# Performance work log

Measured on AMD Instinct MI355X. Metric: run time of the kernel, lower is better.

The kernel has to match this reference:

```python
import jax, jax.numpy as jnp
import numpy as np

N = 100000   # nodes
E = 800000   # edges
FEAT = 384   # raw feature dim (match layer input)
IN = 64      # in_dim
H = 64       # hidden_dim


def setup_inputs() -> dict:
    key = jax.random.key(0)
    ks = jax.random.split(key, 9)
    x = jax.random.normal(ks[0], (N, FEAT), dtype=jnp.float32)
    edge_index = jax.random.randint(ks[1], (2, E), 0, N)
    edge_weight = jax.random.uniform(ks[2], (E,), dtype=jnp.float32)
    Wm = jax.random.normal(ks[3], (FEAT, IN), dtype=jnp.float32) * (FEAT ** -0.5)
    bm = jnp.zeros((IN,), dtype=jnp.float32)
    W1 = jax.random.normal(ks[4], (IN, H), dtype=jnp.float32) * (IN ** -0.5)
    b1 = jnp.zeros((H,), dtype=jnp.float32)
    W2 = jax.random.normal(ks[5], (H, H), dtype=jnp.float32) * (H ** -0.5)
    b2 = jnp.zeros((H,), dtype=jnp.float32)
    return {"x": x, "edge_index": edge_index, "edge_weight": edge_weight,
            "Wm": Wm, "bm": bm, "W1": W1, "b1": b1, "W2": W2, "b2": b2}


def _gcn_conv(x, W, b, src, dst, ew, num_nodes):
    """PyG GCNConv: out = D^{-1/2} (A+I) D^{-1/2} (x W) + b."""
    # add self loops with weight 1
    loop = jnp.arange(num_nodes, dtype=src.dtype)
    row = jnp.concatenate([src, loop])          # source (message sender)
    col = jnp.concatenate([dst, loop])          # destination (aggregation target)
    w = jnp.concatenate([ew, jnp.ones((num_nodes,), dtype=x.dtype)])
    # symmetric normalization: deg computed over destination
    deg = jax.ops.segment_sum(w, col, num_segments=num_nodes)
    dinv = jnp.where(deg > 0, jax.lax.rsqrt(deg), 0.0)
    norm = dinv[row] * w * dinv[col]            # [E+N]
    h = x @ W                                   # [N, out]
    msg = h[row] * norm[:, None]                # gather + scale
    out = jax.ops.segment_sum(msg, col, num_segments=num_nodes)  # scatter-add
    return out + b


def reference(x, edge_index, edge_weight, Wm, bm, W1, b1, W2, b2):
    src, dst = edge_index[0], edge_index[1]
    if x.shape[-1] != IN:
        x = x @ Wm + bm                         # match: Linear(384, in_dim)
    h = _gcn_conv(x, W1, b1, src, dst, edge_weight, N)
    h = jax.nn.relu(h)                          # relu between layers only
    out = _gcn_conv(h, W2, b2, src, dst, edge_weight, N)
    return out
```

## Files before the change

kernel.cpp:

```cpp
#include <hip/hip_runtime.h>


#define NN 100000
#define NE 800000
#define BC 32

typedef unsigned short u16;
typedef __attribute__((ext_vector_type(8))) short short8;
typedef __attribute__((ext_vector_type(4))) float f4;
typedef __attribute__((ext_vector_type(8))) unsigned short u16x8;

__device__ __forceinline__ u16 f2b(float f) {
    unsigned int x = __float_as_uint(f);
    x += 0x7fffu + ((x >> 16) & 1u);
    return (u16)(x >> 16);
}
__device__ __forceinline__ float b2f(u16 u) {
    return __uint_as_float(((unsigned int)u) << 16);
}

__global__ __launch_bounds__(256) void mega_k(const int* __restrict__ ei,
                                              const float* __restrict__ ew,
                                              float* __restrict__ deg,
                                              int* __restrict__ count,
                                              int2* __restrict__ e2,
                                              const float* __restrict__ x,
                                              const float* __restrict__ Wm,
                                              const float* __restrict__ bm,
                                              float* __restrict__ t32) {
    __shared__ u16 Blds[4 * 256 * 8];
    int tid = threadIdx.x, bid = blockIdx.x;
    if (bid < 3125) {
        int e = bid * 256 + tid;
        int src = ei[e];
        int dst = ei[NE + e];
        float wv = ew[e];
        atomicAdd(&deg[dst], wv);
        int pos = atomicAdd(&count[dst], 1);
        if (pos < BC)
            e2[(size_t)dst * BC + pos] = make_int2(src, __float_as_int(wv));
        return;
    }
    int wave = tid >> 6, lane = tid & 63;
    int rowtile = (bid - 3125) * 4 + wave;
    bool act = rowtile < 6250;
    int rowbase = (act ? rowtile : 6249) * 16;
    int m = lane & 15, quad = lane >> 4;

    f4 acc[4];
#pragma unroll
    for (int ct = 0; ct < 4; ct++) acc[ct] = 0.0f;
    const short8* Bfrag = (const short8*)Blds;

#pragma unroll
    for (int chunk = 0; chunk < 3; chunk++) {
        for (int idx = tid; idx < 4 * 256; idx += 256) {
            int ktl = idx >> 8, rem = idx & 255;
            int ct = rem >> 6, ln = rem & 63;
            int kb = (chunk * 4 + ktl) * 32 + (ln >> 4) * 8;
            int col = ct * 16 + (ln & 15);
#pragma unroll
            for (int j = 0; j < 8; j++)
                Blds[idx * 8 + j] = f2b(Wm[(size_t)(kb + j) * 64 + col]);
        }
        __syncthreads();
#pragma unroll
        for (int ktl = 0; ktl < 4; ktl++) {
            const f4* p = (const f4*)&x[(size_t)(rowbase + m) * 384 + (chunk * 4 + ktl) * 32 + quad * 8];
            f4 v0 = p[0], v1 = p[1];
            short8 af;
#pragma unroll
            for (int j = 0; j < 4; j++) {
                af[j]     = (short)f2b(v0[j]);
                af[4 + j] = (short)f2b(v1[j]);
            }
#pragma unroll
            for (int ct = 0; ct < 4; ct++)
                acc[ct] = __builtin_amdgcn_mfma_f32_16x16x32_bf16(af, Bfrag[(ktl * 4 + ct) * 64 + lane], acc[ct], 0, 0, 0);
        }
        __syncthreads();
    }

    if (act) {
#pragma unroll
        for (int ct = 0; ct < 4; ct++) {
            int col = ct * 16 + m;
            float bmv = bm[col];
#pragma unroll
            for (int r = 0; r < 4; r++)
                t32[(size_t)(rowbase + quad * 4 + r) * 64 + col] = acc[ct][r] + bmv;
        }
    }
}

__global__ __launch_bounds__(256) void scale_k(const float* __restrict__ deg,
                                               const float* __restrict__ t32,
                                               u16* __restrict__ ts) {
    int tid = threadIdx.x;
    int rt = tid >> 3, ch = tid & 7;
    int row = blockIdx.x * 32 + rt;
    float rsd = rsqrtf(deg[row] + 1.0f);
    const f4* p = (const f4*)&t32[(size_t)row * 64 + ch * 8];
    f4 v0 = p[0], v1 = p[1];
    u16x8 o;
#pragma unroll
    for (int j = 0; j < 4; j++) {
        o[j]     = f2b(rsd * v0[j]);
        o[4 + j] = f2b(rsd * v1[j]);
    }
    ((u16x8*)ts)[(size_t)row * 8 + ch] = o;
}

__device__ __forceinline__ void gatherR(const int2* __restrict__ eb, int cntv, int dst,
                                        const u16* __restrict__ hb, int ch,
                                        float* __restrict__ acc) {
    const int4* eb4 = (const int4*)eb;
    for (int i = 0; i < cntv; i += 8) {
        int4 q[4];
#pragma unroll
        for (int p = 0; p < 4; p++) q[p] = eb4[(i >> 1) + p];
        int s[8];
        float c[8];
#pragma unroll
        for (int p = 0; p < 4; p++) {
            int t0 = i + 2 * p;
            bool v0 = t0 < cntv, v1 = (t0 + 1) < cntv;
            s[2 * p]     = v0 ? q[p].x : dst;
            c[2 * p]     = v0 ? __int_as_float(q[p].y) : 0.0f;
            s[2 * p + 1] = v1 ? q[p].z : dst;
            c[2 * p + 1] = v1 ? __int_as_float(q[p].w) : 0.0f;
        }
        u16x8 hv[8];
#pragma unroll
        for (int t = 0; t < 8; t++)
            hv[t] = *(const u16x8*)&hb[(size_t)s[t] * 64 + ch * 8];
#pragma unroll
        for (int t = 0; t < 8; t++) {
#pragma unroll
            for (int j = 0; j < 8; j++)
                acc[j] = fmaf(c[t], b2f(hv[t][j]), acc[j]);
        }
    }
}

__device__ __forceinline__ void fillW(u16* Wlds, const float* __restrict__ W, int tid) {
    for (int idx = tid; idx < 2 * 256; idx += 256) {
        int kt = idx >> 8, rem = idx & 255;
        int ct = rem >> 6, ln = rem & 63;
        int kb = kt * 32 + (ln >> 4) * 8;
        int col = ct * 16 + (ln & 15);
#pragma unroll
        for (int j = 0; j < 8; j++)
            Wlds[idx * 8 + j] = f2b(W[(size_t)(kb + j) * 64 + col]);
    }
}

__global__ __launch_bounds__(256) void g1gemm_k(const int2* __restrict__ e2,
                                                const int* __restrict__ count,
                                                const float* __restrict__ deg,
                                                const u16* __restrict__ ts,
                                                const float* __restrict__ W1,
                                                const float* __restrict__ b1,
                                                u16* __restrict__ aggb) {
    __shared__ u16 Wlds[4096];
    __shared__ u16 Atile[32][72];
    __shared__ float rsds[32];
    int tid = threadIdx.x;
    fillW(Wlds, W1, tid);

    int rt = tid >> 3, ch = tid & 7;
    int dst = blockIdx.x * 32 + rt;
    int cntv = min(count[dst], BC);
    float rsdd = rsqrtf(deg[dst] + 1.0f);
    u16x8 hs = *(const u16x8*)&ts[(size_t)dst * 64 + ch * 8];

    float acc[8] = {0, 0, 0, 0, 0, 0, 0, 0};
    gatherR(&e2[(size_t)dst * BC], cntv, dst, ts, ch, acc);

    u16x8 o;
#pragma unroll
    for (int j = 0; j < 8; j++)
        o[j] = f2b(rsdd * (acc[j] + b2f(hs[j])));
    *(u16x8*)&Atile[rt][ch * 8] = o;
    if (ch == 0) rsds[rt] = rsdd;
    __syncthreads();

    if (tid >= 128) return;
    int wave = tid >> 6, lane = tid & 63;
    int m = lane & 15, quad = lane >> 4;
    int rowoff = wave * 16;
    f4 cacc[4];
#pragma unroll
    for (int ct = 0; ct < 4; ct++) cacc[ct] = 0.0f;
    const short8* Bfrag = (const short8*)Wlds;
#pragma unroll
    for (int kt = 0; kt < 2; kt++) {
        short8 af = *(const short8*)&Atile[rowoff + m][kt * 32 + quad * 8];
#pragma unroll
        for (int ct = 0; ct < 4; ct++)
            cacc[ct] = __builtin_amdgcn_mfma_f32_16x16x32_bf16(af, Bfrag[(kt * 4 + ct) * 64 + lane], cacc[ct], 0, 0, 0);
    }
    int rowbase = blockIdx.x * 32 + rowoff;
#pragma unroll
    for (int ct = 0; ct < 4; ct++) {
        int col = ct * 16 + m;
        float bb = b1[col];
#pragma unroll
        for (int rr = 0; rr < 4; rr++) {
            int rl = rowoff + quad * 4 + rr;
            float v = fmaxf(cacc[ct][rr] + bb, 0.0f);
            aggb[(size_t)(rowbase + quad * 4 + rr) * 64 + col] = f2b(rsds[rl] * v);
        }
    }
}

__global__ __launch_bounds__(256) void g2gemm_k(const int2* __restrict__ e2,
                                                const int* __restrict__ count,
                                                const float* __restrict__ deg,
                                                const u16* __restrict__ aggb,
                                                const float* __restrict__ W2,
                                                const float* __restrict__ b2,
                                                float* __restrict__ out) {
    __shared__ u16 Wlds[4096];
    __shared__ u16 Atile[32][72];
    int tid = threadIdx.x;
    fillW(Wlds, W2, tid);

    int rt = tid >> 3, ch = tid & 7;
    int dst = blockIdx.x * 32 + rt;
    int cntv = min(count[dst], BC);
    float rsdd = rsqrtf(deg[dst] + 1.0f);
    u16x8 hs = *(const u16x8*)&aggb[(size_t)dst * 64 + ch * 8];

    float acc[8] = {0, 0, 0, 0, 0, 0, 0, 0};
    gatherR(&e2[(size_t)dst * BC], cntv, dst, aggb, ch, acc);

    u16x8 o;
#pragma unroll
    for (int j = 0; j < 8; j++)
        o[j] = f2b(rsdd * (acc[j] + b2f(hs[j])));
    *(u16x8*)&Atile[rt][ch * 8] = o;
    __syncthreads();

    if (tid >= 128) return;
    int wave = tid >> 6, lane = tid & 63;
    int m = lane & 15, quad = lane >> 4;
    int rowoff = wave * 16;
    f4 cacc[4];
#pragma unroll
    for (int ct = 0; ct < 4; ct++) cacc[ct] = 0.0f;
    const short8* Bfrag = (const short8*)Wlds;
#pragma unroll
    for (int kt = 0; kt < 2; kt++) {
        short8 af = *(const short8*)&Atile[rowoff + m][kt * 32 + quad * 8];
#pragma unroll
        for (int ct = 0; ct < 4; ct++)
            cacc[ct] = __builtin_amdgcn_mfma_f32_16x16x32_bf16(af, Bfrag[(kt * 4 + ct) * 64 + lane], cacc[ct], 0, 0, 0);
    }
    int rowbase = blockIdx.x * 32 + rowoff;
#pragma unroll
    for (int ct = 0; ct < 4; ct++) {
        int col = ct * 16 + m;
        float bc = b2[col];
#pragma unroll
        for (int rr = 0; rr < 4; rr++)
            out[(size_t)(rowbase + quad * 4 + rr) * 64 + col] = cacc[ct][rr] + bc;
    }
}

extern "C" void kernel_launch(void* const* d_in, const int* in_sizes, int n_in,
                              void* d_out, int out_size, void* d_ws, size_t ws_size,
                              hipStream_t stream) {
    const float* x  = (const float*)d_in[0];
    const int*   ei = (const int*)d_in[1];
    const float* ew = (const float*)d_in[2];
    const float* Wm = (const float*)d_in[3];
    const float* bm = (const float*)d_in[4];
    const float* W1 = (const float*)d_in[5];
    const float* b1 = (const float*)d_in[6];
    const float* W2 = (const float*)d_in[7];
    const float* b2 = (const float*)d_in[8];
    float* out = (float*)d_out;

    char*  w     = (char*)d_ws;
    float* deg   = (float*)(w);
    int*   count = (int*)(w + 400000);
    int2*  e2    = (int2*)(w + (4u << 20));
    float* t32   = (float*)(w + (32u << 20));
    u16*   ts    = (u16*)(w + (64u << 20));
    u16*   aggb  = (u16*)(w + (80u << 20));

    hipMemsetAsync(w, 0, 800000, stream);
    mega_k<<<4688, 256, 0, stream>>>(ei, ew, deg, count, e2, x, Wm, bm, t32);
    scale_k<<<3125, 256, 0, stream>>>(deg, t32, ts);
    g1gemm_k<<<3125, 256, 0, stream>>>(e2, count, deg, ts, W1, b1, aggb);
    g2gemm_k<<<3125, 256, 0, stream>>>(e2, count, deg, aggb, W2, b2, out);
}
```

Before: 389.1 us.

## Fuse degree scaling into input GEMM and split edge preprocessing into its own kernel

Edge preprocessing (degree accumulation and CSR-like bucket fill) moves into its own kernel, with the degree atomics and the bucket atomics handled by separate block ranges. The input-projection GEMM now runs after it, so it can apply the rsqrt(deg+1) scaling and bf16 conversion in its epilogue. This drops the scale_k kernel and the fp32 intermediate t32 round trip. The cost is that the GEMM no longer overlaps with the edge atomics inside one launch. Edge arrays are also read twice, and the epilogue writes scattered 2-byte stores.

Result: slower. 398.2 us (+2.3%).

```diff
diff --git a/kernel.cpp b/kernel.cpp
--- a/kernel.cpp
+++ b/kernel.cpp
@@ -19,30 +19,34 @@
     return __uint_as_float(((unsigned int)u) << 16);
 }
 
-__global__ __launch_bounds__(256) void mega_k(const int* __restrict__ ei,
-                                              const float* __restrict__ ew,
-                                              float* __restrict__ deg,
-                                              int* __restrict__ count,
-                                              int2* __restrict__ e2,
-                                              const float* __restrict__ x,
-                                              const float* __restrict__ Wm,
-                                              const float* __restrict__ bm,
-                                              float* __restrict__ t32) {
-    __shared__ u16 Blds[4 * 256 * 8];
+__global__ __launch_bounds__(256) void degfill_k(const int* __restrict__ ei,
+                                                 const float* __restrict__ ew,
+                                                 float* __restrict__ deg,
+                                                 int* __restrict__ count,
+                                                 int2* __restrict__ e2) {
     int tid = threadIdx.x, bid = blockIdx.x;
     if (bid < 3125) {
         int e = bid * 256 + tid;
-        int src = ei[e];
-        int dst = ei[NE + e];
-        float wv = ew[e];
-        atomicAdd(&deg[dst], wv);
-        int pos = atomicAdd(&count[dst], 1);
-        if (pos < BC)
-            e2[(size_t)dst * BC + pos] = make_int2(src, __float_as_int(wv));
+        atomicAdd(&deg[ei[NE + e]], ew[e]);
         return;
     }
+    int e = (bid - 3125) * 256 + tid;
+    int src = ei[e];
+    int dst = ei[NE + e];
+    int pos = atomicAdd(&count[dst], 1);
+    if (pos < BC)
+        e2[(size_t)dst * BC + pos] = make_int2(src, __float_as_int(ew[e]));
+}
+
+__global__ __launch_bounds__(256) void gemmscale_k(const float* __restrict__ x,
+                                                   const float* __restrict__ Wm,
+                                                   const float* __restrict__ bm,
+                                                   const float* __restrict__ deg,
+                                                   u16* __restrict__ ts) {
+    __shared__ u16 Blds[4 * 256 * 8];
+    int tid = threadIdx.x, bid = blockIdx.x;
     int wave = tid >> 6, lane = tid & 63;
-    int rowtile = (bid - 3125) * 4 + wave;
+    int rowtile = bid * 4 + wave;
     bool act = rowtile < 6250;
     int rowbase = (act ? rowtile : 6249) * 16;
     int m = lane & 15, quad = lane >> 4;
@@ -82,33 +86,19 @@
     }
 
     if (act) {
+        float rsd[4];
+#pragma unroll
+        for (int r = 0; r < 4; r++)
+            rsd[r] = rsqrtf(deg[rowbase + quad * 4 + r] + 1.0f);
 #pragma unroll
         for (int ct = 0; ct < 4; ct++) {
             int col = ct * 16 + m;
             float bmv = bm[col];
 #pragma unroll
             for (int r = 0; r < 4; r++)
-                t32[(size_t)(rowbase + quad * 4 + r) * 64 + col] = acc[ct][r] + bmv;
-        }
-    }
-}
-
-__global__ __launch_bounds__(256) void scale_k(const float* __restrict__ deg,
-                                               const float* __restrict__ t32,
-                                               u16* __restrict__ ts) {
-    int tid = threadIdx.x;
-    int rt = tid >> 3, ch = tid & 7;
-    int row = blockIdx.x * 32 + rt;
-    float rsd = rsqrtf(deg[row] + 1.0f);
-    const f4* p = (const f4*)&t32[(size_t)row * 64 + ch * 8];
-    f4 v0 = p[0], v1 = p[1];
-    u16x8 o;
-#pragma unroll
-    for (int j = 0; j < 4; j++) {
-        o[j]     = f2b(rsd * v0[j]);
-        o[4 + j] = f2b(rsd * v1[j]);
-    }
-    ((u16x8*)ts)[(size_t)row * 8 + ch] = o;
+                ts[(size_t)(rowbase + quad * 4 + r) * 64 + col] = f2b(rsd[r] * (acc[ct][r] + bmv));
+        }
+    }
 }
 
 __device__ __forceinline__ void gatherR(const int2* __restrict__ eb, int cntv, int dst,
@@ -286,13 +276,12 @@
     float* deg   = (float*)(w);
     int*   count = (int*)(w + 400000);
     int2*  e2    = (int2*)(w + (4u << 20));
-    float* t32   = (float*)(w + (32u << 20));
-    u16*   ts    = (u16*)(w + (64u << 20));
-    u16*   aggb  = (u16*)(w + (80u << 20));
+    u16*   ts    = (u16*)(w + (32u << 20));
+    u16*   aggb  = (u16*)(w + (48u << 20));
 
     hipMemsetAsync(w, 0, 800000, stream);
-    mega_k<<<4688, 256, 0, stream>>>(ei, ew, deg, count, e2, x, Wm, bm, t32);
-    scale_k<<<3125, 256, 0, stream>>>(deg, t32, ts);
+    degfill_k<<<6250, 256, 0, stream>>>(ei, ew, deg, count, e2);
+    gemmscale_k<<<1563, 256, 0, stream>>>(x, Wm, bm, deg, ts);
     g1gemm_k<<<3125, 256, 0, stream>>>(e2, count, deg, ts, W1, b1, aggb);
     g2gemm_k<<<3125, 256, 0, stream>>>(e2, count, deg, aggb, W2, b2, out);
 }
```
